# Performance work log

Measured on AMD Instinct MI355X. Metric: run time of the kernel, lower is better.

Reference implementation:

```python
import jax, jax.numpy as jnp
import numpy as np
import math

N0 = 50000      # nodes at level 0
E0 = 800000     # edges at level 0 (fixed edge buffer, masked when pooled)
D = 128         # hidden_dim == latent_dim
L = 2           # args.mpl_layers
NB = 2          # args.num_blocks (SAGEConvs per block)
RATIO = 0.5     # args.mpl_ratio
EPS = 1e-12


def setup_inputs() -> dict:
    key = jax.random.key(0)
    ks = jax.random.split(key, 6)
    x = jax.random.normal(ks[0], (N0, D), jnp.float32)
    edge_index = jax.random.randint(ks[1], (2, E0), 0, N0, jnp.int32)
    n_convs = (2 * L + 1) * NB  # down(4) + bottom(2) + up(4) = 10
    Wl = jax.random.normal(ks[2], (n_convs, D, D), jnp.float32) * 0.05
    bl = jax.random.normal(ks[3], (n_convs, D), jnp.float32) * 0.05
    Wr = jax.random.normal(ks[4], (n_convs, D, D), jnp.float32) * 0.05
    pool_p = jax.random.normal(ks[5], (L, D), jnp.float32)
    return {"x": x, "edge_index": edge_index, "Wl": Wl, "bl": bl, "Wr": Wr,
            "pool_p": pool_p}


def _sage(x, src, dst, valid, W_l, b_l, W_r, n):
    """PyG SAGEConv (mean aggr): lin_l(mean_{j->i} x_j) + lin_r(x_i).
    Invalid (masked) edges contribute neither to the sum nor the count."""
    msg = x[src] * valid[:, None]                       # [E, D]
    s = jax.ops.segment_sum(msg, dst, num_segments=n)   # [n, D]
    cnt = jax.ops.segment_sum(valid, dst, num_segments=n)
    mean = s / jnp.maximum(cnt, 1.0)[:, None]
    return mean @ W_l.T + b_l + x @ W_r.T


def _cal_ew(w, src, dst, valid, n):
    """WeightedEdgeConv.cal_ew (no_grad in original)."""
    deg = jax.ops.segment_sum(valid, src, num_segments=n)
    normed = w / jnp.where(deg > 0, deg, 1.0)
    w_send = normed[src] * valid
    aggr_w = jax.ops.segment_sum(w_send, dst, num_segments=n) + EPS
    ec = w_send / aggr_w[dst]
    return jax.lax.stop_gradient(ec), jax.lax.stop_gradient(aggr_w)


def _econv(x, src, dst, ec, n, aggregating=True):
    """WeightedEdgeConv.forward: gather -> scale by edge weight -> scatter-add."""
    if aggregating:
        return jax.ops.segment_sum(x[src] * ec[:, None], dst, num_segments=n)
    return jax.ops.segment_sum(x[dst] * ec[:, None], src, num_segments=n)


def reference(x, edge_index, Wl, bl, Wr, pool_p):
    src, dst = edge_index[0], edge_index[1]
    valid = jnp.ones((E0,), x.dtype)
    n = N0
    conv = 0
    down_outs, down_edges, ecs, perms, sizes = [], [], [], [], []
    w = jnp.ones((N0,), x.dtype)  # b_data.weights (ones by default)

    # ---- down path ----
    for l in range(L):
        for _ in range(NB):
            x = _sage(x, src, dst, valid, Wl[conv], bl[conv], Wr[conv], n)
            conv += 1
        down_outs.append(x)
        down_edges.append((src, dst, valid))
        sizes.append(n)
        ec, w = _cal_ew(w, src, dst, valid, n)
        ecs.append(ec)
        x = _econv(x, src, dst, ec, n, aggregating=True)
        # TopKPooling: score = x.p/||p||, keep top ceil(ratio*n), gate by tanh
        p = pool_p[l]
        score = x @ p / jnp.linalg.norm(p)
        k = int(math.ceil(RATIO * n))
        vals, perm = jax.lax.top_k(score, k)
        x = x[perm] * jnp.tanh(vals)[:, None]
        w = w[perm]
        new_id = jnp.full((n,), -1, jnp.int32).at[perm].set(
            jnp.arange(k, dtype=jnp.int32))
        src2, dst2 = new_id[src], new_id[dst]
        keep = ((src2 >= 0) & (dst2 >= 0)).astype(x.dtype)
        valid = valid * keep
        src = jnp.maximum(src2, 0)
        dst = jnp.maximum(dst2, 0)
        perms.append(perm)
        n = k

    # ---- bottom ----
    for _ in range(NB):
        x = _sage(x, src, dst, valid, Wl[conv], bl[conv], Wr[conv], n)
        conv += 1

    # ---- up path ----
    for i in range(L):
        u = L - 1 - i
        src, dst, valid = down_edges[u]
        n = sizes[u]
        # Unpool: scatter into zeros at kept-node indices
        x = jnp.zeros((n, x.shape[-1]), x.dtype).at[perms[u]].set(x)
        x = _econv(x, src, dst, ecs[u], n, aggregating=False)
        for _ in range(NB):
            x = _sage(x, src, dst, valid, Wl[conv], bl[conv], Wr[conv], n)
            conv += 1
        x = x + down_outs[u]  # skip connection
    return x
```

## Files before the change

kernel.cpp:

```cpp
#include <hip/hip_runtime.h>
#include <stdint.h>

#define DEV __device__ __forceinline__

constexpr int N0 = 50000;
constexpr int E0 = 800000;
constexpr int D  = 128;

typedef __attribute__((ext_vector_type(8))) short bf16x8;
typedef __attribute__((ext_vector_type(4))) float f32x4;

DEV float bf2f(unsigned u) { return __uint_as_float(u << 16); }
DEV unsigned short f2bf(float f) {
  unsigned u = __float_as_uint(f);
  unsigned r = u + 0x7fffu + ((u >> 16) & 1u);
  return (unsigned short)(r >> 16);
}

DEV unsigned wave_incl_scan(unsigned v, int lane) {
  #pragma unroll
  for (int off = 1; off < 64; off <<= 1) {
    unsigned u = __shfl_up(v, (unsigned)off);
    if (lane >= off) v += u;
  }
// ... 8 lines not shown
    rank_src[e] = atomicAdd(&cnt_src[src[e]], 1u);
    rank_dst[e] = atomicAdd(&cnt_dst[dst[e]], 1u);
  }
}

__global__ void k_psum(const unsigned* __restrict__ in, int n, unsigned* __restrict__ part) {
  int t = threadIdx.x, lane = t & 63, w = t >> 6;
  int base = blockIdx.x * 1024 + t * 4;
  unsigned s = 0;
  #pragma unroll
  for (int j = 0; j < 4; ++j) { int i = base + j; if (i < n) s += in[i]; }
  #pragma unroll
  for (int off = 32; off >= 1; off >>= 1) s += __shfl_xor(s, off);
  __shared__ unsigned ws[4];
  if (lane == 0) ws[w] = s;
  __syncthreads();
  if (t == 0) part[blockIdx.x] = ws[0] + ws[1] + ws[2] + ws[3];
}

__global__ void k_scoff(const unsigned* __restrict__ part, int nch,
                        unsigned* __restrict__ off, unsigned* __restrict__ total_out) {
  if (threadIdx.x == 0) {
    unsigned run = 0;
    for (int c = 0; c < nch; ++c) { off[c] = run; run += part[c]; }
    *total_out = run;
  }
}

__global__ void k_sapply(const unsigned* __restrict__ in, const unsigned* __restrict__ choff,
                         int n, unsigned* __restrict__ out) {
  int t = threadIdx.x, lane = t & 63, w = t >> 6;
  int base = blockIdx.x * 1024 + t * 4;
  unsigned v[4]; unsigned s = 0;
  #pragma unroll
  for (int j = 0; j < 4; ++j) { int i = base + j; v[j] = (i < n) ? in[i] : 0u; s += v[j]; }
  unsigned incl = wave_incl_scan(s, lane);
  __shared__ unsigned wsum[4], woff[4];
  if (lane == 63) wsum[w] = incl;
  __syncthreads();
  if (t == 0) { unsigned run = 0; for (int j = 0; j < 4; ++j) { woff[j] = run; run += wsum[j]; } }
  __syncthreads();
  unsigned run = choff[blockIdx.x] + woff[w] + incl - s;
  #pragma unroll
  for (int j = 0; j < 4; ++j) {
    int i = base + j;
    if (i < n) out[i] = run;
    run += v[j];
  }
}

__global__ void k_fill2(const int* __restrict__ src, const int* __restrict__ dst,
                        const unsigned* __restrict__ rank_src, const unsigned* __restrict__ rank_dst,
                        const unsigned* __restrict__ indptr_src, const unsigned* __restrict__ indptr_dst,
                        int* __restrict__ adj_src, int* __restrict__ adj_dst) {
  int e = blockIdx.x * blockDim.x + threadIdx.x;
  if (e < E0) {
    int s = src[e], d = dst[e];
    adj_dst[indptr_dst[d] + rank_dst[e]] = s;
    adj_src[indptr_src[s] + rank_src[e]] = d;
  }
}

__global__ void k_adj_next2(const int* __restrict__ adjd, const int* __restrict__ adjs,
                            const int* __restrict__ new_id,
                            int* __restrict__ outd, int* __restrict__ outs) {
  int pos = blockIdx.x * blockDim.x + threadIdx.x;
  if (pos < E0) {
    int a = adjd[pos];
    outd[pos] = (a >= 0) ? new_id[a] : -1;
    int b = adjs[pos];
    outs[pos] = (b >= 0) ? new_id[b] : -1;
  }
}

__global__ void k_adj_next(const int* __restrict__ adj_prev, const int* __restrict__ new_id,
                           int* __restrict__ adj_out) {
  int pos = blockIdx.x * blockDim.x + threadIdx.x;
  if (pos < E0) {
    int a = adj_prev[pos];
    adj_out[pos] = (a >= 0) ? new_id[a] : -1;
  }
}

__global__ void k_wt(const float* __restrict__ Wl, const float* __restrict__ Wr, float* __restrict__ BT) {
  int idx = blockIdx.x * blockDim.x + threadIdx.x;
  if (idx < 4 * 256 * 128) {
    int o = idx & 127;
    int k = (idx >> 7) & 255;
    int c = idx >> 15;
    float v = (k < 128) ? Wl[(c * 128 + o) * 128 + k] : Wr[(c * 128 + o) * 128 + (k - 128)];
    BT[idx] = v;
  }
}

__global__ void k_wt_pk(const float* __restrict__ Wl, const float* __restrict__ Wr,
                        unsigned short* __restrict__ Bhi, unsigned short* __restrict__ Blo) {
  int idx = blockIdx.x * blockDim.x + threadIdx.x;
  if (idx >= 6 * 8 * 8 * 64) return;
  int l  = idx & 63;
  int ct = (idx >> 6) & 7;
  int ks = (idx >> 9) & 7;
  int c  = idx >> 12;
  int k0 = ks * 32 + (l >> 4) * 8;
  int o  = ct * 16 + (l & 15);
  int conv = c + 4;
  const float* Wrow = (k0 < 128) ? (Wl + ((size_t)conv * 128 + o) * 128 + k0)
                                 : (Wr + ((size_t)conv * 128 + o) * 128 + (k0 - 128));
  size_t base = (size_t)idx * 8;
  #pragma unroll
  for (int j = 0; j < 8; ++j) {
    float wv = Wrow[j];
    unsigned short h = f2bf(wv);
    Bhi[base + j] = h;
    Blo[base + j] = f2bf(wv - bf2f(h));
  }
}

template<bool BF, bool MASKED>
__global__ void k_sage(const void* __restrict__ xv, const int* __restrict__ adj,
                       const unsigned* __restrict__ indptr, const int* __restrict__ orig,
                       int n, float* __restrict__ mean) {
  int wid = (blockIdx.x * blockDim.x + threadIdx.x) >> 6;
  int lane = threadIdx.x & 63;
  if (wid >= n) return;
  int o = orig ? orig[wid] : wid;
  unsigned s0 = indptr[o], s1 = indptr[o + 1];
  const float* xf = (const float*)xv;
  const unsigned* xb = (const unsigned*)xv;
  float a0 = 0.f, a1 = 0.f, cnt = 0.f;
  unsigned idx = s0;
  for (; idx + 4 <= s1; idx += 4) {
    int ad[4];
    #pragma unroll
    for (int j = 0; j < 4; ++j) ad[j] = adj[idx + j];
    #pragma unroll
    for (int j = 0; j < 4; ++j) {
      if (!MASKED || ad[j] >= 0) {
        float x0, x1;
        if (BF) { unsigned u = xb[(size_t)ad[j] * 64 + lane]; x0 = bf2f(u & 0xffffu); x1 = bf2f(u >> 16); }
        else    { float2 v = *(const float2*)(xf + (size_t)ad[j] * D + lane * 2); x0 = v.x; x1 = v.y; }
        a0 += x0; a1 += x1; cnt += 1.f;
      }
    }
  }
  for (; idx < s1; ++idx) {
    int a = adj[idx];
    if (!MASKED || a >= 0) {
      float x0, x1;
      if (BF) { unsigned u = xb[(size_t)a * 64 + lane]; x0 = bf2f(u & 0xffffu); x1 = bf2f(u >> 16); }
      else    { float2 v = *(const float2*)(xf + (size_t)a * D + lane * 2); x0 = v.x; x1 = v.y; }
      a0 += x0; a1 += x1; cnt += 1.f;
    }
  }
  if (!MASKED) cnt = (float)(s1 - s0);
  float inv = 1.0f / fmaxf(cnt, 1.0f);
  *(float2*)(mean + (size_t)wid * D + lane * 2) = make_float2(a0 * inv, a1 * inv);
}

template<bool BF, bool MASKED>
__global__ void k_econv2(const void* __restrict__ xv, const int* __restrict__ adj,
                         const float* __restrict__ ecs, const unsigned* __restrict__ indptr,
                         const int* __restrict__ orig, int n,
                         float* __restrict__ out, unsigned* __restrict__ outbf) {
  int wid = (blockIdx.x * blockDim.x + threadIdx.x) >> 6;
  int lane = threadIdx.x & 63;
  if (wid >= n) return;
  int o = orig ? orig[wid] : wid;
  unsigned s0 = indptr[o], s1 = indptr[o + 1];
  const float* xf = (const float*)xv;
  const unsigned* xb = (const unsigned*)xv;
  float a0 = 0.f, a1 = 0.f;
  unsigned idx = s0;
  for (; idx + 4 <= s1; idx += 4) {
    int ad[4]; float wv[4];
    #pragma unroll
    for (int j = 0; j < 4; ++j) { ad[j] = adj[idx + j]; wv[j] = ecs[idx + j]; }
    #pragma unroll
    for (int j = 0; j < 4; ++j) {
      if (!MASKED || ad[j] >= 0) {
        float x0, x1;
        if (BF) { unsigned u = xb[(size_t)ad[j] * 64 + lane]; x0 = bf2f(u & 0xffffu); x1 = bf2f(u >> 16); }
        else    { float2 v = *(const float2*)(xf + (size_t)ad[j] * D + lane * 2); x0 = v.x; x1 = v.y; }
        a0 = fmaf(wv[j], x0, a0); a1 = fmaf(wv[j], x1, a1);
      }
    }
  }
  for (; idx < s1; ++idx) {
    int a = adj[idx]; float wgt = ecs[idx];
    if (!MASKED || a >= 0) {
      float x0, x1;
      if (BF) { unsigned u = xb[(size_t)a * 64 + lane]; x0 = bf2f(u & 0xffffu); x1 = bf2f(u >> 16); }
      else    { float2 v = *(const float2*)(xf + (size_t)a * D + lane * 2); x0 = v.x; x1 = v.y; }
      a0 = fmaf(wgt, x0, a0); a1 = fmaf(wgt, x1, a1);
    }
  }
  *(float2*)(out + (size_t)wid * D + lane * 2) = make_float2(a0, a1);
  if (outbf) {
    unsigned p = (unsigned)f2bf(a0) | ((unsigned)f2bf(a1) << 16);
    outbf[(size_t)wid * 64 + lane] = p;
  }
}

__launch_bounds__(256)
__global__ void k_conv_gemm(const float* __restrict__ mean, const float* __restrict__ xin,
                            const float* __restrict__ BT, const float* __restrict__ bias,
                            float* __restrict__ y, unsigned short* __restrict__ ybf, int n) {
  __shared__ float As[64][17];
  __shared__ float Bs[16][128];
  int tid = threadIdx.x;
  int tx = tid & 15, ty = tid >> 4;
  int row0 = blockIdx.x * 64;
  float acc[4][8];
  #pragma unroll
  for (int r = 0; r < 4; ++r)
    #pragma unroll
    for (int c = 0; c < 8; ++c) acc[r][c] = 0.f;

  int lm = tid >> 2;
  int lk = (tid & 3) * 4;
  int bk = tid >> 4;
  int bo = (tid & 15) * 8;

  for (int kc = 0; kc < 16; ++kc) {
    int k0 = kc * 16;
    const float* A = (k0 < 128) ? mean : xin;
    int kk = k0 & 127;
    int gr = row0 + lm;
    float4 av = make_float4(0.f, 0.f, 0.f, 0.f);
    if (gr < n) av = *(const float4*)(A + (size_t)gr * D + kk + lk);
    As[lm][lk + 0] = av.x; As[lm][lk + 1] = av.y; As[lm][lk + 2] = av.z; As[lm][lk + 3] = av.w;
    float4 bv0 = *(const float4*)(BT + (size_t)(k0 + bk) * 128 + bo);
    float4 bv1 = *(const float4*)(BT + (size_t)(k0 + bk) * 128 + bo + 4);
    *(float4*)&Bs[bk][bo] = bv0;
    *(float4*)&Bs[bk][bo + 4] = bv1;
    __syncthreads();
    #pragma unroll
    for (int k = 0; k < 16; ++k) {
      float a[4];
      #pragma unroll
      for (int r = 0; r < 4; ++r) a[r] = As[ty * 4 + r][k];
      float4 b0 = *(const float4*)&Bs[k][tx * 4];
      float4 b1 = *(const float4*)&Bs[k][64 + tx * 4];
      float bb[8] = {b0.x, b0.y, b0.z, b0.w, b1.x, b1.y, b1.z, b1.w};
      #pragma unroll
      for (int r = 0; r < 4; ++r)
        #pragma unroll
        for (int c = 0; c < 8; ++c)
          acc[r][c] = fmaf(a[r], bb[c], acc[r][c]);
    }
    __syncthreads();
  }
  float4 bs0 = *(const float4*)(bias + tx * 4);
  float4 bs1 = *(const float4*)(bias + 64 + tx * 4);
  #pragma unroll
  for (int r = 0; r < 4; ++r) {
    int gr = row0 + ty * 4 + r;
    if (gr < n) {
      float4 o0 = make_float4(acc[r][0] + bs0.x, acc[r][1] + bs0.y, acc[r][2] + bs0.z, acc[r][3] + bs0.w);
      float4 o1 = make_float4(acc[r][4] + bs1.x, acc[r][5] + bs1.y, acc[r][6] + bs1.z, acc[r][7] + bs1.w);
      *(float4*)(y + (size_t)gr * D + tx * 4) = o0;
      *(float4*)(y + (size_t)gr * D + 64 + tx * 4) = o1;
      if (ybf) {
        ushort4 p0; p0.x = f2bf(o0.x); p0.y = f2bf(o0.y); p0.z = f2bf(o0.z); p0.w = f2bf(o0.w);
        ushort4 p1; p1.x = f2bf(o1.x); p1.y = f2bf(o1.y); p1.z = f2bf(o1.z); p1.w = f2bf(o1.w);
        *(ushort4*)(ybf + (size_t)gr * D + tx * 4) = p0;
        *(ushort4*)(ybf + (size_t)gr * D + 64 + tx * 4) = p1;
      }
    }
  }
}

__launch_bounds__(256)
__global__ void k_gemm_mfma(const float* __restrict__ mean, const float* __restrict__ xin,
                            const unsigned short* __restrict__ Bhi, const unsigned short* __restrict__ Blo,
                            const float* __restrict__ bias, const float* __restrict__ skip,
                            float* __restrict__ y, unsigned short* __restrict__ ybf, int n) {
  int tid = threadIdx.x;
  int lane = tid & 63, w = tid >> 6;
  int row0 = blockIdx.x * 64 + w * 16;
  int arow = row0 + (lane & 15);
  int kgrp = lane >> 4;
  bool rowok = arow < n;
  f32x4 acc[8];
  #pragma unroll
  for (int ct = 0; ct < 8; ++ct) acc[ct] = f32x4{0.f, 0.f, 0.f, 0.f};

  #pragma unroll
  for (int ks = 0; ks < 8; ++ks) {
    const float* A = (ks < 4) ? mean : xin;
    int kk = (ks & 3) * 32 + kgrp * 8;
    float av[8];
    if (rowok) {
      float4 a0 = *(const float4*)(A + (size_t)arow * D + kk);
      float4 a1 = *(const float4*)(A + (size_t)arow * D + kk + 4);
      av[0] = a0.x; av[1] = a0.y; av[2] = a0.z; av[3] = a0.w;
      av[4] = a1.x; av[5] = a1.y; av[6] = a1.z; av[7] = a1.w;
    } else {
      #pragma unroll
      for (int j = 0; j < 8; ++j) av[j] = 0.f;
    }
    bf16x8 ahi, alo;
    #pragma unroll
    for (int j = 0; j < 8; ++j) {
      unsigned short h = f2bf(av[j]);
      ahi[j] = (short)h;
      alo[j] = (short)f2bf(av[j] - bf2f(h));
    }
    #pragma unroll
    for (int ct = 0; ct < 8; ++ct) {
      size_t boff = (((size_t)ks * 8 + ct) * 64 + lane) * 8;
      bf16x8 bh = *(const bf16x8*)(Bhi + boff);
      bf16x8 bl = *(const bf16x8*)(Blo + boff);
      acc[ct] = __builtin_amdgcn_mfma_f32_16x16x32_bf16(ahi, bh, acc[ct], 0, 0, 0);
      acc[ct] = __builtin_amdgcn_mfma_f32_16x16x32_bf16(alo, bh, acc[ct], 0, 0, 0);
      acc[ct] = __builtin_amdgcn_mfma_f32_16x16x32_bf16(ahi, bl, acc[ct], 0, 0, 0);
    }
  }
  int ccol = lane & 15;
  #pragma unroll
  for (int ct = 0; ct < 8; ++ct) {
    int col = ct * 16 + ccol;
    float bb = bias[col];
    #pragma unroll
    for (int r = 0; r < 4; ++r) {
      int row = row0 + kgrp * 4 + r;
      if (row < n) {
        float v = acc[ct][r] + bb;
        if (skip) v += skip[(size_t)row * D + col];
        y[(size_t)row * D + col] = v;
        if (ybf) ybf[(size_t)row * D + col] = f2bf(v);
      }
    }
  }
}

__global__ void k_deg_len(const unsigned* __restrict__ indptr, int n, float* __restrict__ deg) {
  int j = blockIdx.x * blockDim.x + threadIdx.x;
  if (j < n) deg[j] = (float)(indptr[j + 1] - indptr[j]);
}

__global__ void k_deg_mask(const int* __restrict__ adj_src, const unsigned* __restrict__ indptr_src,
                           const int* __restrict__ orig, int n, float* __restrict__ deg) {
  int j = blockIdx.x * blockDim.x + threadIdx.x;
  if (j >= n) return;
  int o = orig ? orig[j] : j;
  unsigned s0 = indptr_src[o], s1 = indptr_src[o + 1];
  float d = 0.f;
  for (unsigned i = s0; i < s1; ++i) d += (adj_src[i] >= 0) ? 1.f : 0.f;
  deg[j] = d;
}

template<bool MASKED>
__global__ void k_ew_dst(const int* __restrict__ adj, const unsigned* __restrict__ indptr,
                         const int* __restrict__ orig, const float* __restrict__ w,
                         const float* __restrict__ deg, int n,
                         float* __restrict__ ws_slot, float* __restrict__ aggrw,
                         float* __restrict__ ec_slot) {
  int j = blockIdx.x * blockDim.x + threadIdx.x;
  if (j >= n) return;
  int o = orig ? orig[j] : j;
  unsigned s0 = indptr[o], s1 = indptr[o + 1];
  float s = 1e-12f;
  for (unsigned pos = s0; pos < s1; ++pos) {
    int a = adj[pos];
    float ws = 0.f;
    if (!MASKED || a >= 0) {
      float d = deg[a];
      ws = (w ? w[a] : 1.0f) / (d > 0.f ? d : 1.0f);
    }
    ws_slot[pos] = ws;
    s += ws;
  }
  aggrw[j] = s;
  float inv = 1.0f / s;
  for (unsigned pos = s0; pos < s1; ++pos) ec_slot[pos] = ws_slot[pos] * inv;
}

template<bool MASKED>
__global__ void k_ew_src(const int* __restrict__ adj_src, const unsigned* __restrict__ indptr_src,
                         const int* __restrict__ orig, const float* __restrict__ w,
                         const float* __restrict__ deg, const float* __restrict__ aggrw, int n,
                         float* __restrict__ ec_slot) {
  int j = blockIdx.x * blockDim.x + threadIdx.x;
  if (j >= n) return;
  int o = orig ? orig[j] : j;
  unsigned s0 = indptr_src[o], s1 = indptr_src[o + 1];
  float d = deg[j];
  float wn = (w ? w[j] : 1.0f) / (d > 0.f ? d : 1.0f);
  for (unsigned pos = s0; pos < s1; ++pos) {
    int a = adj_src[pos];
    ec_slot[pos] = (!MASKED || a >= 0) ? (wn / aggrw[a]) : 0.f;
  }
}

DEV unsigned mono_key(float f) {
  unsigned u = __float_as_uint(f);
  return (u & 0x80000000u) ? ~u : (u | 0x80000000u);
}

__global__ void k_score(const float* __restrict__ x, const float* __restrict__ p,
                        int n, float* __restrict__ score, unsigned* __restrict__ keys) {
  int wid = (blockIdx.x * blockDim.x + threadIdx.x) >> 6;
  int lane = threadIdx.x & 63;
  if (wid >= n) return;
  float p0 = p[lane * 2], p1 = p[lane * 2 + 1];
  const float2 xv = *(const float2*)(x + (size_t)wid * D + lane * 2);
  float partial = xv.x * p0 + xv.y * p1;
  float pn = p0 * p0 + p1 * p1;
  #pragma unroll
  for (int off = 32; off >= 1; off >>= 1) {
    partial += __shfl_xor(partial, off);
    pn += __shfl_xor(pn, off);
  }
  if (lane == 0) {
    float sc = partial * (1.0f / sqrtf(pn));
    score[wid] = sc;
    keys[wid] = mono_key(sc);
  }
}

__global__ void k_sel_init(unsigned* bins, unsigned* state, int k) {
  int t = threadIdx.x;
  if (t < 256) bins[t] = 0u;
  if (t == 0) { state[0] = 0u; state[1] = (unsigned)k; }
}

__global__ void k_hist(const unsigned* __restrict__ keys, int n, const unsigned* __restrict__ state,
                       unsigned* __restrict__ bins, int byte) {
  __shared__ unsigned lb[256];
  for (int i = threadIdx.x; i < 256; i += blockDim.x) lb[i] = 0u;
  __syncthreads();
  unsigned prefix = state[0];
  unsigned mask = (byte == 3) ? 0u : (0xFFFFFFFFu << ((byte + 1) * 8));
  for (int i = blockIdx.x * blockDim.x + threadIdx.x; i < n; i += gridDim.x * blockDim.x) {
    unsigned key = keys[i];
    if ((key & mask) == (prefix & mask))
      atomicAdd(&lb[(key >> (byte * 8)) & 255], 1u);
  }
  __syncthreads();
  for (int i = threadIdx.x; i < 256; i += blockDim.x)
    if (lb[i]) atomicAdd(&bins[i], lb[i]);
}

__global__ void k_pick(unsigned* bins, unsigned* state, int byte) {
  if (threadIdx.x == 0) {
    unsigned r = state[1];
    int b;
    for (b = 255; b > 0; --b) {
      unsigned c = bins[b];
      if (c >= r) break;
      r -= c;
    }
    state[0] |= ((unsigned)b) << (byte * 8);
    state[1] = r;
  }
  __syncthreads();
  for (int i = threadIdx.x; i < 256; i += blockDim.x) bins[i] = 0u;
}

__global__ void k_flags(const unsigned* __restrict__ keys, const unsigned* __restrict__ state,
                        int n, uint2* __restrict__ part) {
  int t = threadIdx.x, lane = t & 63, w = t >> 6;
  int base = blockIdx.x * 1024 + t * 4;
  unsigned T = state[0];
  unsigned cnt = 0;
  #pragma unroll
  for (int j = 0; j < 4; ++j) {
    int i = base + j;
    if (i < n) {
      unsigned key = keys[i];
// ... 77 lines not shown
  float2 v = *(const float2*)(xin + (size_t)j * D + lane * 2);
  v.x *= g; v.y *= g;
  *(float2*)(xout + (size_t)wid * D + lane * 2) = v;
  if (outbf) {
    unsigned p = (unsigned)f2bf(v.x) | ((unsigned)f2bf(v.y) << 16);
    outbf[(size_t)wid * 64 + lane] = p;
  }
}

__global__ void k_scatter_bf(const float* __restrict__ xin, const int* __restrict__ perm,
                             int k, unsigned* __restrict__ outbf) {
  int wid = (blockIdx.x * blockDim.x + threadIdx.x) >> 6;
  int lane = threadIdx.x & 63;
  if (wid >= k) return;
  int p = perm[wid];
  float2 v = *(const float2*)(xin + (size_t)wid * D + lane * 2);
  unsigned pk = (unsigned)f2bf(v.x) | ((unsigned)f2bf(v.y) << 16);
  outbf[(size_t)p * 64 + lane] = pk;
}

extern "C" void kernel_launch(void* const* d_in, const int* in_sizes, int n_in,
                              void* d_out, int out_size, void* d_ws, size_t ws_size,
                              hipStream_t stream) {
  const float* x_in   = (const float*)d_in[0];
  const int*   ei     = (const int*)d_in[1];
  const int*   src0   = ei;
  const int*   dst0   = ei + E0;
  const float* Wl     = (const float*)d_in[2];
  const float* bl     = (const float*)d_in[3];
  const float* Wr     = (const float*)d_in[4];
  const float* pool_p = (const float*)d_in[5];
  float* out = (float*)d_out;

  const int n0 = N0, k0 = 25000, n1 = 25000, k1 = 12500, n2 = 12500;
  const int NCH0 = (N0 + 1023) / 1024;

  char* ws = (char*)d_ws;
  size_t off = 0;
  auto alloc = [&](size_t bytes) -> char* {
    char* p = ws + off;
    off += (bytes + 255) & ~(size_t)255;
    return p;
  };
  const size_t NBY = (size_t)N0 * D * 4;
  float* B0    = (float*)alloc(NBY);
  float* B1    = (float*)alloc(NBY);
  float* B2    = (float*)alloc(NBY);
  float* down0 = (float*)alloc(NBY);
  float* down1 = (float*)alloc(NBY / 2);
  unsigned* MA = (unsigned*)alloc((size_t)N0 * D * 2);
  unsigned* MB = (unsigned*)alloc((size_t)N0 * D * 2);
  int* adj0_dst = (int*)alloc(E0 * 4);
  int* adj0_src = (int*)alloc(E0 * 4);
  int* adj1_dst = (int*)alloc(E0 * 4);
  int* adj1_src = (int*)alloc(E0 * 4);
  float* ec0_src = (float*)alloc(E0 * 4);
  float* ec1_src = (float*)alloc(E0 * 4);
  float* ec_dst  = (float*)alloc(E0 * 4);
  float* ws_slot = (float*)alloc(E0 * 4);
  int* adj2_dst  = (int*)ws_slot;
  unsigned* rank_src = (unsigned*)alloc(E0 * 4);
  unsigned* rank_dst = (unsigned*)alloc(E0 * 4);
  unsigned* indptr_dst = (unsigned*)alloc((N0 + 1) * 4);
  unsigned* indptr_src = (unsigned*)alloc((N0 + 1) * 4);
  unsigned* cnt_src = (unsigned*)alloc(N0 * 4);
  unsigned* cnt_dst = (unsigned*)alloc(N0 * 4);
  float* deg   = (float*)alloc(N0 * 4);
  float* aggrw = (float*)alloc(N0 * 4);
  float* w1 = (float*)alloc(n1 * 4);
  float* w2 = (float*)alloc(n2 * 4);
  float* score = (float*)alloc(N0 * 4);
  unsigned* keys = (unsigned*)alloc(N0 * 4);
  int* perm0 = (int*)alloc(k0 * 4);
  int* perm1 = (int*)alloc(k1 * 4);
  int* orig1 = (int*)alloc(k0 * 4);
  int* orig2 = (int*)alloc(k1 * 4);
  int* new_id = (int*)alloc(N0 * 4);
  unsigned* bins  = (unsigned*)alloc(256 * 4);
  unsigned* state = (unsigned*)alloc(8);
  unsigned* spart = (unsigned*)alloc(64 * 4);
  unsigned* soff  = (unsigned*)alloc(64 * 4);
  uint2* ppart = (uint2*)alloc(64 * 8);
  uint2* poff  = (uint2*)alloc(64 * 8);
  float* BT = (float*)alloc((size_t)4 * 256 * 128 * 4);
  unsigned short* Bhi = (unsigned short*)alloc((size_t)6 * 8 * 8 * 64 * 8 * 2);
  unsigned short* Blo = (unsigned short*)alloc((size_t)6 * 8 * 8 * 64 * 8 * 2);

  const int EG = (E0 + 255) / 256;

  auto scan_np1 = [&](const unsigned* in, unsigned* outp, int n, int nch) {
    k_psum<<<nch, 256, 0, stream>>>(in, n, spart);
    k_scoff<<<1, 64, 0, stream>>>(spart, nch, soff, outp + n);
    k_sapply<<<nch, 256, 0, stream>>>(in, soff, n, outp);
  };

  hipMemsetAsync(cnt_src, 0, N0 * 4, stream);
  hipMemsetAsync(cnt_dst, 0, N0 * 4, stream);
  k_count<<<EG, 256, 0, stream>>>(src0, dst0, cnt_src, cnt_dst, rank_src, rank_dst);
  scan_np1(cnt_src, indptr_src, N0, NCH0);
  scan_np1(cnt_dst, indptr_dst, N0, NCH0);
  k_fill2<<<EG, 256, 0, stream>>>(src0, dst0, rank_src, rank_dst, indptr_src, indptr_dst,
                                  adj0_src, adj0_dst);
  k_wt<<<(4 * 256 * 128 + 255) / 256, 256, 0, stream>>>(Wl, Wr, BT);
  k_wt_pk<<<(6 * 8 * 8 * 64 + 255) / 256, 256, 0, stream>>>(Wl, Wr, Bhi, Blo);

  auto gemm = [&](const float* meanb, const float* xin, float* yout, unsigned short* ybf,
                  int n, int cidx) {
    k_conv_gemm<<<(n + 63) / 64, 256, 0, stream>>>(meanb, xin, BT + (size_t)cidx * 256 * 128,
                                                   bl + cidx * 128, yout, ybf, n);
  };
  auto gemm_mx = [&](const float* meanb, const float* xin, float* yout, unsigned short* ybf,
                     const float* skip, int n, int cidx) {
    size_t o = (size_t)(cidx - 4) * 8 * 8 * 64 * 8;
    k_gemm_mfma<<<(n + 63) / 64, 256, 0, stream>>>(meanb, xin, Bhi + o, Blo + o,
                                                   bl + cidx * 128, skip, yout, ybf, n);
  };

  auto pool_sel = [&](const float* xpool, int n, int kk, int level, const int* orig,
                      int* perm, float* w_next, int* orig_next,
                      float* xout, unsigned* xout_bf) {
    int nch = (n + 1023) / 1024;
    k_score<<<(n + 3) / 4, 256, 0, stream>>>(xpool, pool_p + level * D, n, score, keys);
    k_sel_init<<<1, 256, 0, stream>>>(bins, state, kk);
    for (int byte = 3; byte >= 0; --byte) {
      k_hist<<<256, 256, 0, stream>>>(keys, n, state, bins, byte);
      k_pick<<<1, 256, 0, stream>>>(bins, state, byte);
    }
    k_flags<<<nch, 256, 0, stream>>>(keys, state, n, ppart);
    k_choff<<<1, 64, 0, stream>>>(ppart, nch, poff);
    k_pack2<<<nch, 256, 0, stream>>>(keys, state, poff, aggrw, orig, n, perm, new_id, w_next, orig_next);
    k_gate<<<(kk + 3) / 4, 256, 0, stream>>>(xpool, perm, score, kk, xout, xout_bf);
  };

  k_sage<false, false><<<(n0 + 3) / 4, 256, 0, stream>>>(x_in, adj0_dst, indptr_dst, nullptr, n0, B1);
  gemm(B1, x_in, B2, nullptr, n0, 0);
  k_sage<false, false><<<(n0 + 3) / 4, 256, 0, stream>>>(B2, adj0_dst, indptr_dst, nullptr, n0, B1);
  gemm(B1, B2, down0, nullptr, n0, 1);
  k_deg_len<<<(n0 + 255) / 256, 256, 0, stream>>>(indptr_src, n0, deg);
  k_ew_dst<false><<<(n0 + 255) / 256, 256, 0, stream>>>(adj0_dst, indptr_dst, nullptr, nullptr, deg, n0,
                                                        ws_slot, aggrw, ec_dst);
  k_ew_src<false><<<(n0 + 255) / 256, 256, 0, stream>>>(adj0_src, indptr_src, nullptr, nullptr, deg, aggrw,
                                                        n0, ec0_src);
  k_econv2<false, false><<<(n0 + 3) / 4, 256, 0, stream>>>(down0, adj0_dst, ec_dst, indptr_dst, nullptr,
                                                           n0, B1, nullptr);
  pool_sel(B1, n0, k0, 0, nullptr, perm0, w1, orig1, B2, nullptr);
  k_adj_next2<<<EG, 256, 0, stream>>>(adj0_dst, adj0_src, new_id, adj1_dst, adj1_src);

  k_sage<false, true><<<(n1 + 3) / 4, 256, 0, stream>>>(B2, adj1_dst, indptr_dst, orig1, n1, B1);
  gemm(B1, B2, B0, nullptr, n1, 2);
  k_sage<false, true><<<(n1 + 3) / 4, 256, 0, stream>>>(B0, adj1_dst, indptr_dst, orig1, n1, B1);
  gemm(B1, B0, down1, nullptr, n1, 3);
  k_deg_mask<<<(n1 + 255) / 256, 256, 0, stream>>>(adj1_src, indptr_src, orig1, n1, deg);
  k_ew_dst<true><<<(n1 + 255) / 256, 256, 0, stream>>>(adj1_dst, indptr_dst, orig1, w1, deg, n1,
                                                       ws_slot, aggrw, ec_dst);
  k_ew_src<true><<<(n1 + 255) / 256, 256, 0, stream>>>(adj1_src, indptr_src, orig1, w1, deg, aggrw,
                                                       n1, ec1_src);
  k_econv2<false, true><<<(n1 + 3) / 4, 256, 0, stream>>>(down1, adj1_dst, ec_dst, indptr_dst, orig1,
                                                          n1, B1, nullptr);
  pool_sel(B1, n1, k1, 1, orig1, perm1, w2, orig2, B2, MA);
  k_adj_next<<<EG, 256, 0, stream>>>(adj1_dst, new_id, adj2_dst);

  k_sage<true, true><<<(n2 + 3) / 4, 256, 0, stream>>>(MA, adj2_dst, indptr_dst, orig2, n2, B1);
  gemm_mx(B1, B2, B0, (unsigned short*)MB, nullptr, n2, 4);
  k_sage<true, true><<<(n2 + 3) / 4, 256, 0, stream>>>(MB, adj2_dst, indptr_dst, orig2, n2, B1);
  gemm_mx(B1, B0, B2, nullptr, nullptr, n2, 5);

  hipMemsetAsync(MA, 0, (size_t)n1 * D * 2, stream);
  k_scatter_bf<<<(n2 + 3) / 4, 256, 0, stream>>>(B2, perm1, n2, MA);
  k_econv2<true, true><<<(n1 + 3) / 4, 256, 0, stream>>>(MA, adj1_src, ec1_src, indptr_src, orig1,
                                                         n1, B1, MB);
  k_sage<true, true><<<(n1 + 3) / 4, 256, 0, stream>>>(MB, adj1_dst, indptr_dst, orig1, n1, B0);
  gemm_mx(B0, B1, B2, (unsigned short*)MA, nullptr, n1, 6);
  k_sage<true, true><<<(n1 + 3) / 4, 256, 0, stream>>>(MA, adj1_dst, indptr_dst, orig1, n1, B0);
  gemm_mx(B0, B2, B1, nullptr, down1, n1, 7);

  hipMemsetAsync(MA, 0, (size_t)n0 * D * 2, stream);
  k_scatter_bf<<<(n1 + 3) / 4, 256, 0, stream>>>(B1, perm0, n1, MA);
  k_econv2<true, false><<<(n0 + 3) / 4, 256, 0, stream>>>(MA, adj0_src, ec0_src, indptr_src, nullptr,
                                                          n0, B2, MB);
  k_sage<true, false><<<(n0 + 3) / 4, 256, 0, stream>>>(MB, adj0_dst, indptr_dst, nullptr, n0, B1);
  gemm_mx(B1, B2, B0, (unsigned short*)MA, nullptr, n0, 8);
  k_sage<true, false><<<(n0 + 3) / 4, 256, 0, stream>>>(MA, adj0_dst, indptr_dst, nullptr, n0, B1);
  gemm_mx(B1, B0, out, nullptr, down0, n0, 9);
}
```

Measured before the change: 1.192 ms.

## Use split-bf16 MFMA GEMM for down path and widen gather loads

Replaces the fp32 FMA tiled GEMM used by the first four convolutions with an MFMA kernel that splits both operands into three bf16 parts and runs six products, which keeps near-fp32 accuracy while using the matrix cores. The gather/mean and edge-weighted aggregation kernels are rewritten so each wave processes several edges at once with wider float4/uint4 loads, followed by cross-lane shuffle reductions. The separate degree kernel is folded into the edge-weight kernels, and weight packing is unified into a three-part split for all ten convs. The six MFMAs per tile add compute and the A operand is split on the fly, and the gather loops now carry partial sums that must be reduced across lanes.

```diff
diff --git a/kernel.cpp b/kernel.cpp
--- a/kernel.cpp
+++ b/kernel.cpp
@@ -114,190 +114,207 @@
   }
 }
 
-__global__ void k_wt(const float* __restrict__ Wl, const float* __restrict__ Wr, float* __restrict__ BT) {
+__global__ void k_wt_pk3(const float* __restrict__ Wl, const float* __restrict__ Wr,
+                         unsigned short* __restrict__ Bh, unsigned short* __restrict__ Bm,
+                         unsigned short* __restrict__ Bl) {
   int idx = blockIdx.x * blockDim.x + threadIdx.x;
-  if (idx < 4 * 256 * 128) {
-    int o = idx & 127;
-    int k = (idx >> 7) & 255;
-    int c = idx >> 15;
-    float v = (k < 128) ? Wl[(c * 128 + o) * 128 + k] : Wr[(c * 128 + o) * 128 + (k - 128)];
-    BT[idx] = v;
-  }
-}
-
-__global__ void k_wt_pk(const float* __restrict__ Wl, const float* __restrict__ Wr,
-                        unsigned short* __restrict__ Bhi, unsigned short* __restrict__ Blo) {
-  int idx = blockIdx.x * blockDim.x + threadIdx.x;
-  if (idx >= 6 * 8 * 8 * 64) return;
+  if (idx >= 10 * 8 * 8 * 64) return;
   int l  = idx & 63;
   int ct = (idx >> 6) & 7;
   int ks = (idx >> 9) & 7;
   int c  = idx >> 12;
   int k0 = ks * 32 + (l >> 4) * 8;
   int o  = ct * 16 + (l & 15);
-  int conv = c + 4;
-  const float* Wrow = (k0 < 128) ? (Wl + ((size_t)conv * 128 + o) * 128 + k0)
-                                 : (Wr + ((size_t)conv * 128 + o) * 128 + (k0 - 128));
+  const float* Wrow = (k0 < 128) ? (Wl + ((size_t)c * 128 + o) * 128 + k0)
+                                 : (Wr + ((size_t)c * 128 + o) * 128 + (k0 - 128));
   size_t base = (size_t)idx * 8;
   #pragma unroll
   for (int j = 0; j < 8; ++j) {
     float wv = Wrow[j];
     unsigned short h = f2bf(wv);
-    Bhi[base + j] = h;
-    Blo[base + j] = f2bf(wv - bf2f(h));
-  }
-}
-
-template<bool BF, bool MASKED>
-__global__ void k_sage(const void* __restrict__ xv, const int* __restrict__ adj,
-                       const unsigned* __restrict__ indptr, const int* __restrict__ orig,
-                       int n, float* __restrict__ mean) {
+    float r1 = wv - bf2f(h);
+    unsigned short m = f2bf(r1);
+    float r2 = r1 - bf2f(m);
+    Bh[base + j] = h;
+    Bm[base + j] = m;
+    Bl[base + j] = f2bf(r2);
+  }
+}
+
+template<bool MEAN, bool MASKED, bool ECW>
+__global__ void k_gf32(const float* __restrict__ x, const int* __restrict__ adj,
+                       const float* __restrict__ ecs, const unsigned* __restrict__ indptr,
+                       const int* __restrict__ orig, int n, float* __restrict__ out) {
   int wid = (blockIdx.x * blockDim.x + threadIdx.x) >> 6;
   int lane = threadIdx.x & 63;
   if (wid >= n) return;
   int o = orig ? orig[wid] : wid;
   unsigned s0 = indptr[o], s1 = indptr[o + 1];
-  const float* xf = (const float*)xv;
-  const unsigned* xb = (const unsigned*)xv;
-  float a0 = 0.f, a1 = 0.f, cnt = 0.f;
-  unsigned idx = s0;
-  for (; idx + 4 <= s1; idx += 4) {
-    int ad[4];
-    #pragma unroll
-    for (int j = 0; j < 4; ++j) ad[j] = adj[idx + j];
+  int half = lane >> 5, sl = lane & 31;
+  float a0 = 0.f, a1 = 0.f, a2 = 0.f, a3 = 0.f, cnt = 0.f;
+  for (unsigned idx = s0; idx < s1; idx += 8) {
     #pragma unroll
     for (int j = 0; j < 4; ++j) {
-      if (!MASKED || ad[j] >= 0) {
-        float x0, x1;
-        if (BF) { unsigned u = xb[(size_t)ad[j] * 64 + lane]; x0 = bf2f(u & 0xffffu); x1 = bf2f(u >> 16); }
-        else    { float2 v = *(const float2*)(xf + (size_t)ad[j] * D + lane * 2); x0 = v.x; x1 = v.y; }
-        a0 += x0; a1 += x1; cnt += 1.f;
+      unsigned e = idx + j * 2 + half;
+      if (e < s1) {
+        int a = adj[e];
+        if (!MASKED || a >= 0) {
+          const float4 v = *(const float4*)(x + (size_t)a * D + sl * 4);
+          if (ECW) {
+            float w = ecs[e];
+            a0 = fmaf(w, v.x, a0); a1 = fmaf(w, v.y, a1);
+            a2 = fmaf(w, v.z, a2); a3 = fmaf(w, v.w, a3);
+          } else {
+            a0 += v.x; a1 += v.y; a2 += v.z; a3 += v.w;
+          }
+          cnt += 1.f;
+        }
       }
     }
   }
-  for (; idx < s1; ++idx) {
-    int a = adj[idx];
-    if (!MASKED || a >= 0) {
-      float x0, x1;
-      if (BF) { unsigned u = xb[(size_t)a * 64 + lane]; x0 = bf2f(u & 0xffffu); x1 = bf2f(u >> 16); }
-      else    { float2 v = *(const float2*)(xf + (size_t)a * D + lane * 2); x0 = v.x; x1 = v.y; }
-      a0 += x0; a1 += x1; cnt += 1.f;
-    }
-  }
-  if (!MASKED) cnt = (float)(s1 - s0);
-  float inv = 1.0f / fmaxf(cnt, 1.0f);
-  *(float2*)(mean + (size_t)wid * D + lane * 2) = make_float2(a0 * inv, a1 * inv);
-}
-
-template<bool BF, bool MASKED>
-__global__ void k_econv2(const void* __restrict__ xv, const int* __restrict__ adj,
-                         const float* __restrict__ ecs, const unsigned* __restrict__ indptr,
-                         const int* __restrict__ orig, int n,
-                         float* __restrict__ out, unsigned* __restrict__ outbf) {
+  a0 += __shfl_xor(a0, 32); a1 += __shfl_xor(a1, 32);
+  a2 += __shfl_xor(a2, 32); a3 += __shfl_xor(a3, 32);
+  if (MEAN) {
+    cnt += __shfl_xor(cnt, 32);
+    if (!MASKED) cnt = (float)(s1 - s0);
+    float inv = 1.0f / fmaxf(cnt, 1.0f);
+    a0 *= inv; a1 *= inv; a2 *= inv; a3 *= inv;
+  }
+  if (half == 0)
+    *(float4*)(out + (size_t)wid * D + sl * 4) = make_float4(a0, a1, a2, a3);
+}
+
+template<bool MEAN, bool MASKED, bool ECW>
+__global__ void k_gbf(const unsigned* __restrict__ xb, const int* __restrict__ adj,
+                      const float* __restrict__ ecs, const unsigned* __restrict__ indptr,
+                      const int* __restrict__ orig, int n,
+                      float* __restrict__ out, unsigned* __restrict__ outbf) {
   int wid = (blockIdx.x * blockDim.x + threadIdx.x) >> 6;
   int lane = threadIdx.x & 63;
   if (wid >= n) return;
   int o = orig ? orig[wid] : wid;
   unsigned s0 = indptr[o], s1 = indptr[o + 1];
-  const float* xf = (const float*)xv;
-  const unsigned* xb = (const unsigned*)xv;
-  float a0 = 0.f, a1 = 0.f;
-  unsigned idx = s0;
-  for (; idx + 4 <= s1; idx += 4) {
-    int ad[4]; float wv[4];
-    #pragma unroll
-    for (int j = 0; j < 4; ++j) { ad[j] = adj[idx + j]; wv[j] = ecs[idx + j]; }
+  int q = lane >> 4, sl = lane & 15;
+  float acc[8];
+  #pragma unroll
+  for (int k = 0; k < 8; ++k) acc[k] = 0.f;
+  float cnt = 0.f;
+  for (unsigned idx = s0; idx < s1; idx += 16) {
     #pragma unroll
     for (int j = 0; j < 4; ++j) {
-      if (!MASKED || ad[j] >= 0) {
-        float x0, x1;
-        if (BF) { unsigned u = xb[(size_t)ad[j] * 64 + lane]; x0 = bf2f(u & 0xffffu); x1 = bf2f(u >> 16); }
-        else    { float2 v = *(const float2*)(xf + (size_t)ad[j] * D + lane * 2); x0 = v.x; x1 = v.y; }
-        a0 = fmaf(wv[j], x0, a0); a1 = fmaf(wv[j], x1, a1);
+      unsigned e = idx + j * 4 + q;
+      if (e < s1) {
+        int a = adj[e];
+        if (!MASKED || a >= 0) {
+          const uint4 v = *(const uint4*)(xb + (size_t)a * 64 + sl * 4);
+          float f0 = bf2f(v.x & 0xffffu), f1 = bf2f(v.x >> 16);
+          float f2 = bf2f(v.y & 0xffffu), f3 = bf2f(v.y >> 16);
+          float f4 = bf2f(v.z & 0xffffu), f5 = bf2f(v.z >> 16);
+          float f6 = bf2f(v.w & 0xffffu), f7 = bf2f(v.w >> 16);
+          if (ECW) {
+            float w = ecs[e];
+            acc[0] = fmaf(w, f0, acc[0]); acc[1] = fmaf(w, f1, acc[1]);
+            acc[2] = fmaf(w, f2, acc[2]); acc[3] = fmaf(w, f3, acc[3]);
+            acc[4] = fmaf(w, f4, acc[4]); acc[5] = fmaf(w, f5, acc[5]);
+            acc[6] = fmaf(w, f6, acc[6]); acc[7] = fmaf(w, f7, acc[7]);
+          } else {
+            acc[0] += f0; acc[1] += f1; acc[2] += f2; acc[3] += f3;
+            acc[4] += f4; acc[5] += f5; acc[6] += f6; acc[7] += f7;
+          }
+          cnt += 1.f;
+        }
       }
     }
   }
-  for (; idx < s1; ++idx) {
-    int a = adj[idx]; float wgt = ecs[idx];
-    if (!MASKED || a >= 0) {
-      float x0, x1;
-      if (BF) { unsigned u = xb[(size_t)a * 64 + lane]; x0 = bf2f(u & 0xffffu); x1 = bf2f(u >> 16); }
-      else    { float2 v = *(const float2*)(xf + (size_t)a * D + lane * 2); x0 = v.x; x1 = v.y; }
-      a0 = fmaf(wgt, x0, a0); a1 = fmaf(wgt, x1, a1);
-    }
-  }
-  *(float2*)(out + (size_t)wid * D + lane * 2) = make_float2(a0, a1);
-  if (outbf) {
-    unsigned p = (unsigned)f2bf(a0) | ((unsigned)f2bf(a1) << 16);
-    outbf[(size_t)wid * 64 + lane] = p;
+  #pragma unroll
+  for (int k = 0; k < 8; ++k) {
+    acc[k] += __shfl_xor(acc[k], 16);
+    acc[k] += __shfl_xor(acc[k], 32);
+  }
+  if (MEAN) {
+    cnt += __shfl_xor(cnt, 16);
+    cnt += __shfl_xor(cnt, 32);
+    if (!MASKED) cnt = (float)(s1 - s0);
+    float inv = 1.0f / fmaxf(cnt, 1.0f);
+    #pragma unroll
+    for (int k = 0; k < 8; ++k) acc[k] *= inv;
+  }
+  if (q == 0) {
+    *(float4*)(out + (size_t)wid * D + sl * 8)     = make_float4(acc[0], acc[1], acc[2], acc[3]);
+    *(float4*)(out + (size_t)wid * D + sl * 8 + 4) = make_float4(acc[4], acc[5], acc[6], acc[7]);
+    if (outbf) {
+      uint4 p;
+      p.x = (unsigned)f2bf(acc[0]) | ((unsigned)f2bf(acc[1]) << 16);
+      p.y = (unsigned)f2bf(acc[2]) | ((unsigned)f2bf(acc[3]) << 16);
+      p.z = (unsigned)f2bf(acc[4]) | ((unsigned)f2bf(acc[5]) << 16);
+      p.w = (unsigned)f2bf(acc[6]) | ((unsigned)f2bf(acc[7]) << 16);
+      *(uint4*)(outbf + (size_t)wid * 64 + sl * 4) = p;
+    }
   }
 }
 
 __launch_bounds__(256)
-__global__ void k_conv_gemm(const float* __restrict__ mean, const float* __restrict__ xin,
-                            const float* __restrict__ BT, const float* __restrict__ bias,
-                            float* __restrict__ y, unsigned short* __restrict__ ybf, int n) {
-  __shared__ float As[64][17];
-  __shared__ float Bs[16][128];
+__global__ void k_gemm_mfma6(const float* __restrict__ mean, const float* __restrict__ xin,
+                             const unsigned short* __restrict__ Bh, const unsigned short* __restrict__ Bm,
+                             const unsigned short* __restrict__ Bl,
+                             const float* __restrict__ bias,
+                             float* __restrict__ y, int n) {
   int tid = threadIdx.x;
-  int tx = tid & 15, ty = tid >> 4;
-  int row0 = blockIdx.x * 64;
-  float acc[4][8];
-  #pragma unroll
-  for (int r = 0; r < 4; ++r)
-    #pragma unroll
-    for (int c = 0; c < 8; ++c) acc[r][c] = 0.f;
-
-  int lm = tid >> 2;
-  int lk = (tid & 3) * 4;
-  int bk = tid >> 4;
-  int bo = (tid & 15) * 8;
-
-  for (int kc = 0; kc < 16; ++kc) {
-    int k0 = kc * 16;
-    const float* A = (k0 < 128) ? mean : xin;
-    int kk = k0 & 127;
-    int gr = row0 + lm;
-    float4 av = make_float4(0.f, 0.f, 0.f, 0.f);
-    if (gr < n) av = *(const float4*)(A + (size_t)gr * D + kk + lk);
-    As[lm][lk + 0] = av.x; As[lm][lk + 1] = av.y; As[lm][lk + 2] = av.z; As[lm][lk + 3] = av.w;
-    float4 bv0 = *(const float4*)(BT + (size_t)(k0 + bk) * 128 + bo);
-    float4 bv1 = *(const float4*)(BT + (size_t)(k0 + bk) * 128 + bo + 4);
-    *(float4*)&Bs[bk][bo] = bv0;
-    *(float4*)&Bs[bk][bo + 4] = bv1;
-    __syncthreads();
-    #pragma unroll
-    for (int k = 0; k < 16; ++k) {
-      float a[4];
+  int lane = tid & 63, w = tid >> 6;
+  int row0 = blockIdx.x * 64 + w * 16;
+  int arow = row0 + (lane & 15);
+  int kgrp = lane >> 4;
+  bool rowok = arow < n;
+  f32x4 acc[8];
+  #pragma unroll
+  for (int ct = 0; ct < 8; ++ct) acc[ct] = f32x4{0.f, 0.f, 0.f, 0.f};
+
+  #pragma unroll
+  for (int ks = 0; ks < 8; ++ks) {
+    const float* A = (ks < 4) ? mean : xin;
+    int kk = (ks & 3) * 32 + kgrp * 8;
+    float av[8];
+    if (rowok) {
+      float4 x0 = *(const float4*)(A + (size_t)arow * D + kk);
+      float4 x1 = *(const float4*)(A + (size_t)arow * D + kk + 4);
+      av[0] = x0.x; av[1] = x0.y; av[2] = x0.z; av[3] = x0.w;
+      av[4] = x1.x; av[5] = x1.y; av[6] = x1.z; av[7] = x1.w;
+    } else {
       #pragma unroll
-      for (int r = 0; r < 4; ++r) a[r] = As[ty * 4 + r][k];
-      float4 b0 = *(const float4*)&Bs[k][tx * 4];
-      float4 b1 = *(const float4*)&Bs[k][64 + tx * 4];
-      float bb[8] = {b0.x, b0.y, b0.z, b0.w, b1.x, b1.y, b1.z, b1.w};
-      #pragma unroll
-      for (int r = 0; r < 4; ++r)
-        #pragma unroll
-        for (int c = 0; c < 8; ++c)
-          acc[r][c] = fmaf(a[r], bb[c], acc[r][c]);
-    }
-    __syncthreads();
-  }
-  float4 bs0 = *(const float4*)(bias + tx * 4);
-  float4 bs1 = *(const float4*)(bias + 64 + tx * 4);
-  #pragma unroll
-  for (int r = 0; r < 4; ++r) {
-    int gr = row0 + ty * 4 + r;
-    if (gr < n) {
-      float4 o0 = make_float4(acc[r][0] + bs0.x, acc[r][1] + bs0.y, acc[r][2] + bs0.z, acc[r][3] + bs0.w);
-      float4 o1 = make_float4(acc[r][4] + bs1.x, acc[r][5] + bs1.y, acc[r][6] + bs1.z, acc[r][7] + bs1.w);
-      *(float4*)(y + (size_t)gr * D + tx * 4) = o0;
-      *(float4*)(y + (size_t)gr * D + 64 + tx * 4) = o1;
-      if (ybf) {
-        ushort4 p0; p0.x = f2bf(o0.x); p0.y = f2bf(o0.y); p0.z = f2bf(o0.z); p0.w = f2bf(o0.w);
-        ushort4 p1; p1.x = f2bf(o1.x); p1.y = f2bf(o1.y); p1.z = f2bf(o1.z); p1.w = f2bf(o1.w);
-        *(ushort4*)(ybf + (size_t)gr * D + tx * 4) = p0;
-        *(ushort4*)(ybf + (size_t)gr * D + 64 + tx * 4) = p1;
-      }
+      for (int j = 0; j < 8; ++j) av[j] = 0.f;
+    }
+    bf16x8 ah, am, al;
+    #pragma unroll
+    for (int j = 0; j < 8; ++j) {
+      unsigned short h = f2bf(av[j]);
+      float r1 = av[j] - bf2f(h);
+      unsigned short m = f2bf(r1);
+      float r2 = r1 - bf2f(m);
+      ah[j] = (short)h; am[j] = (short)m; al[j] = (short)f2bf(r2);
+    }
+    #pragma unroll
+    for (int ct = 0; ct < 8; ++ct) {
+      size_t boff = (((size_t)ks * 8 + ct) * 64 + lane) * 8;
+      bf16x8 bh = *(const bf16x8*)(Bh + boff);
+      bf16x8 bm = *(const bf16x8*)(Bm + boff);
+      bf16x8 bl = *(const bf16x8*)(Bl + boff);
+      acc[ct] = __builtin_amdgcn_mfma_f32_16x16x32_bf16(ah, bh, acc[ct], 0, 0, 0);
+      acc[ct] = __builtin_amdgcn_mfma_f32_16x16x32_bf16(ah, bm, acc[ct], 0, 0, 0);
+      acc[ct] = __builtin_amdgcn_mfma_f32_16x16x32_bf16(am, bh, acc[ct], 0, 0, 0);
+      acc[ct] = __builtin_amdgcn_mfma_f32_16x16x32_bf16(am, bm, acc[ct], 0, 0, 0);
+      acc[ct] = __builtin_amdgcn_mfma_f32_16x16x32_bf16(ah, bl, acc[ct], 0, 0, 0);
+      acc[ct] = __builtin_amdgcn_mfma_f32_16x16x32_bf16(al, bh, acc[ct], 0, 0, 0);
+    }
+  }
+  int ccol = lane & 15;
+  #pragma unroll
+  for (int ct = 0; ct < 8; ++ct) {
+    int col = ct * 16 + ccol;
+    float bb = bias[col];
+    #pragma unroll
+    for (int r = 0; r < 4; ++r) {
+      int row = row0 + kgrp * 4 + r;
+      if (row < n) y[(size_t)row * D + col] = acc[ct][r] + bb;
     }
   }
 }
@@ -323,10 +340,10 @@
     int kk = (ks & 3) * 32 + kgrp * 8;
     float av[8];
     if (rowok) {
-      float4 a0 = *(const float4*)(A + (size_t)arow * D + kk);
-      float4 a1 = *(const float4*)(A + (size_t)arow * D + kk + 4);
-      av[0] = a0.x; av[1] = a0.y; av[2] = a0.z; av[3] = a0.w;
-      av[4] = a1.x; av[5] = a1.y; av[6] = a1.z; av[7] = a1.w;
+      float4 x0 = *(const float4*)(A + (size_t)arow * D + kk);
+      float4 x1 = *(const float4*)(A + (size_t)arow * D + kk + 4);
+      av[0] = x0.x; av[1] = x0.y; av[2] = x0.z; av[3] = x0.w;
+      av[4] = x1.x; av[5] = x1.y; av[6] = x1.z; av[7] = x1.w;
     } else {
       #pragma unroll
       for (int j = 0; j < 8; ++j) av[j] = 0.f;
@@ -364,11 +381,6 @@
       }
     }
   }
-}
-
-__global__ void k_deg_len(const unsigned* __restrict__ indptr, int n, float* __restrict__ deg) {
-  int j = blockIdx.x * blockDim.x + threadIdx.x;
-  if (j < n) deg[j] = (float)(indptr[j + 1] - indptr[j]);
 }
 
 __global__ void k_deg_mask(const int* __restrict__ adj_src, const unsigned* __restrict__ indptr_src,
@@ -384,6 +396,7 @@
 
 template<bool MASKED>
 __global__ void k_ew_dst(const int* __restrict__ adj, const unsigned* __restrict__ indptr,
+                         const unsigned* __restrict__ ips,
                          const int* __restrict__ orig, const float* __restrict__ w,
                          const float* __restrict__ deg, int n,
                          float* __restrict__ ws_slot, float* __restrict__ aggrw,
@@ -397,7 +410,7 @@
     int a = adj[pos];
     float ws = 0.f;
     if (!MASKED || a >= 0) {
-      float d = deg[a];
+      float d = deg ? deg[a] : (float)(ips[a + 1] - ips[a]);
       ws = (w ? w[a] : 1.0f) / (d > 0.f ? d : 1.0f);
     }
     ws_slot[pos] = ws;
@@ -417,7 +430,7 @@
   if (j >= n) return;
   int o = orig ? orig[j] : j;
   unsigned s0 = indptr_src[o], s1 = indptr_src[o + 1];
-  float d = deg[j];
+  float d = deg ? deg[j] : (float)(s1 - s0);
   float wn = (w ? w[j] : 1.0f) / (d > 0.f ? d : 1.0f);
   for (unsigned pos = s0; pos < s1; ++pos) {
     int a = adj_src[pos];
@@ -661,9 +674,9 @@
   unsigned* soff  = (unsigned*)alloc(64 * 4);
   uint2* ppart = (uint2*)alloc(64 * 8);
   uint2* poff  = (uint2*)alloc(64 * 8);
-  float* BT = (float*)alloc((size_t)4 * 256 * 128 * 4);
-  unsigned short* Bhi = (unsigned short*)alloc((size_t)6 * 8 * 8 * 64 * 8 * 2);
-  unsigned short* Blo = (unsigned short*)alloc((size_t)6 * 8 * 8 * 64 * 8 * 2);
+  unsigned short* Bh = (unsigned short*)alloc((size_t)10 * 32768 * 2);
+  unsigned short* Bm = (unsigned short*)alloc((size_t)10 * 32768 * 2);
+  unsigned short* Bl = (unsigned short*)alloc((size_t)10 * 32768 * 2);
 
   const int EG = (E0 + 255) / 256;
 
@@ -680,18 +693,17 @@
   scan_np1(cnt_dst, indptr_dst, N0, NCH0);
   k_fill2<<<EG, 256, 0, stream>>>(src0, dst0, rank_src, rank_dst, indptr_src, indptr_dst,
                                   adj0_src, adj0_dst);
-  k_wt<<<(4 * 256 * 128 + 255) / 256, 256, 0, stream>>>(Wl, Wr, BT);
-  k_wt_pk<<<(6 * 8 * 8 * 64 + 255) / 256, 256, 0, stream>>>(Wl, Wr, Bhi, Blo);
-
-  auto gemm = [&](const float* meanb, const float* xin, float* yout, unsigned short* ybf,
-                  int n, int cidx) {
-    k_conv_gemm<<<(n + 63) / 64, 256, 0, stream>>>(meanb, xin, BT + (size_t)cidx * 256 * 128,
-                                                   bl + cidx * 128, yout, ybf, n);
+  k_wt_pk3<<<(10 * 8 * 8 * 64 + 255) / 256, 256, 0, stream>>>(Wl, Wr, Bh, Bm, Bl);
+
+  auto gemm6 = [&](const float* meanb, const float* xin, float* yout, int n, int cidx) {
+    size_t o = (size_t)cidx * 32768;
+    k_gemm_mfma6<<<(n + 63) / 64, 256, 0, stream>>>(meanb, xin, Bh + o, Bm + o, Bl + o,
+                                                    bl + cidx * 128, yout, n);
   };
   auto gemm_mx = [&](const float* meanb, const float* xin, float* yout, unsigned short* ybf,
                      const float* skip, int n, int cidx) {
-    size_t o = (size_t)(cidx - 4) * 8 * 8 * 64 * 8;
-    k_gemm_mfma<<<(n + 63) / 64, 256, 0, stream>>>(meanb, xin, Bhi + o, Blo + o,
+    size_t o = (size_t)cidx * 32768;
+    k_gemm_mfma<<<(n + 63) / 64, 256, 0, stream>>>(meanb, xin, Bh + o, Bm + o,
                                                    bl + cidx * 128, skip, yout, ybf, n);
   };
 
@@ -711,54 +723,51 @@
     k_gate<<<(kk + 3) / 4, 256, 0, stream>>>(xpool, perm, score, kk, xout, xout_bf);
   };
 
-  k_sage<false, false><<<(n0 + 3) / 4, 256, 0, stream>>>(x_in, adj0_dst, indptr_dst, nullptr, n0, B1);
-  gemm(B1, x_in, B2, nullptr, n0, 0);
-  k_sage<false, false><<<(n0 + 3) / 4, 256, 0, stream>>>(B2, adj0_dst, indptr_dst, nullptr, n0, B1);
-  gemm(B1, B2, down0, nullptr, n0, 1);
-  k_deg_len<<<(n0 + 255) / 256, 256, 0, stream>>>(indptr_src, n0, deg);
-  k_ew_dst<false><<<(n0 + 255) / 256, 256, 0, stream>>>(adj0_dst, indptr_dst, nullptr, nullptr, deg, n0,
-                                                        ws_slot, aggrw, ec_dst);
-  k_ew_src<false><<<(n0 + 255) / 256, 256, 0, stream>>>(adj0_src, indptr_src, nullptr, nullptr, deg, aggrw,
-                                                        n0, ec0_src);
-  k_econv2<false, false><<<(n0 + 3) / 4, 256, 0, stream>>>(down0, adj0_dst, ec_dst, indptr_dst, nullptr,
-                                                           n0, B1, nullptr);
+  const int G0 = (n0 + 3) / 4, G1 = (n1 + 3) / 4, G2 = (n2 + 3) / 4;
+
+  k_gf32<true, false, false><<<G0, 256, 0, stream>>>(x_in, adj0_dst, nullptr, indptr_dst, nullptr, n0, B1);
+  gemm6(B1, x_in, B2, n0, 0);
+  k_gf32<true, false, false><<<G0, 256, 0, stream>>>(B2, adj0_dst, nullptr, indptr_dst, nullptr, n0, B1);
+  gemm6(B1, B2, down0, n0, 1);
+  k_ew_dst<false><<<(n0 + 255) / 256, 256, 0, stream>>>(adj0_dst, indptr_dst, indptr_src, nullptr,
+                                                        nullptr, nullptr, n0, ws_slot, aggrw, ec_dst);
+  k_ew_src<false><<<(n0 + 255) / 256, 256, 0, stream>>>(adj0_src, indptr_src, nullptr, nullptr,
+                                                        nullptr, aggrw, n0, ec0_src);
+  k_gf32<false, false, true><<<G0, 256, 0, stream>>>(down0, adj0_dst, ec_dst, indptr_dst, nullptr, n0, B1);
   pool_sel(B1, n0, k0, 0, nullptr, perm0, w1, orig1, B2, nullptr);
   k_adj_next2<<<EG, 256, 0, stream>>>(adj0_dst, adj0_src, new_id, adj1_dst, adj1_src);
 
-  k_sage<false, true><<<(n1 + 3) / 4, 256, 0, stream>>>(B2, adj1_dst, indptr_dst, orig1, n1, B1);
-  gemm(B1, B2, B0, nullptr, n1, 2);
-  k_sage<false, true><<<(n1 + 3) / 4, 256, 0, stream>>>(B0, adj1_dst, indptr_dst, orig1, n1, B1);
-  gemm(B1, B0, down1, nullptr, n1, 3);
+  k_gf32<true, true, false><<<G1, 256, 0, stream>>>(B2, adj1_dst, nullptr, indptr_dst, orig1, n1, B1);
+  gemm6(B1, B2, B0, n1, 2);
+  k_gf32<true, true, false><<<G1, 256, 0, stream>>>(B0, adj1_dst, nullptr, indptr_dst, orig1, n1, B1);
+  gemm6(B1, B0, down1, n1, 3);
   k_deg_mask<<<(n1 + 255) / 256, 256, 0, stream>>>(adj1_src, indptr_src, orig1, n1, deg);
-  k_ew_dst<true><<<(n1 + 255) / 256, 256, 0, stream>>>(adj1_dst, indptr_dst, orig1, w1, deg, n1,
-                                                       ws_slot, aggrw, ec_dst);
+  k_ew_dst<true><<<(n1 + 255) / 256, 256, 0, stream>>>(adj1_dst, indptr_dst, nullptr, orig1, w1,
+                                                       deg, n1, ws_slot, aggrw, ec_dst);
   k_ew_src<true><<<(n1 + 255) / 256, 256, 0, stream>>>(adj1_src, indptr_src, orig1, w1, deg, aggrw,
                                                        n1, ec1_src);
-  k_econv2<false, true><<<(n1 + 3) / 4, 256, 0, stream>>>(down1, adj1_dst, ec_dst, indptr_dst, orig1,
-                                                          n1, B1, nullptr);
+  k_gf32<false, true, true><<<G1, 256, 0, stream>>>(down1, adj1_dst, ec_dst, indptr_dst, orig1, n1, B1);
   pool_sel(B1, n1, k1, 1, orig1, perm1, w2, orig2, B2, MA);
   k_adj_next<<<EG, 256, 0, stream>>>(adj1_dst, new_id, adj2_dst);
 
-  k_sage<true, true><<<(n2 + 3) / 4, 256, 0, stream>>>(MA, adj2_dst, indptr_dst, orig2, n2, B1);
+  k_gbf<true, true, false><<<G2, 256, 0, stream>>>(MA, adj2_dst, nullptr, indptr_dst, orig2, n2, B1, nullptr);
   gemm_mx(B1, B2, B0, (unsigned short*)MB, nullptr, n2, 4);
-  k_sage<true, true><<<(n2 + 3) / 4, 256, 0, stream>>>(MB, adj2_dst, indptr_dst, orig2, n2, B1);
+  k_gbf<true, true, false><<<G2, 256, 0, stream>>>(MB, adj2_dst, nullptr, indptr_dst, orig2, n2, B1, nullptr);
   gemm_mx(B1, B0, B2, nullptr, nullptr, n2, 5);
 
   hipMemsetAsync(MA, 0, (size_t)n1 * D * 2, stream);
-  k_scatter_bf<<<(n2 + 3) / 4, 256, 0, stream>>>(B2, perm1, n2, MA);
-  k_econv2<true, true><<<(n1 + 3) / 4, 256, 0, stream>>>(MA, adj1_src, ec1_src, indptr_src, orig1,
-                                                         n1, B1, MB);
-  k_sage<true, true><<<(n1 + 3) / 4, 256, 0, stream>>>(MB, adj1_dst, indptr_dst, orig1, n1, B0);
+  k_scatter_bf<<<G2, 256, 0, stream>>>(B2, perm1, n2, MA);
+  k_gbf<false, true, true><<<G1, 256, 0, stream>>>(MA, adj1_src, ec1_src, indptr_src, orig1, n1, B1, MB);
+  k_gbf<true, true, false><<<G1, 256, 0, stream>>>(MB, adj1_dst, nullptr, indptr_dst, orig1, n1, B0, nullptr);
   gemm_mx(B0, B1, B2, (unsigned short*)MA, nullptr, n1, 6);
-  k_sage<true, true><<<(n1 + 3) / 4, 256, 0, stream>>>(MA, adj1_dst, indptr_dst, orig1, n1, B0);
+  k_gbf<true, true, false><<<G1, 256, 0, stream>>>(MA, adj1_dst, nullptr, indptr_dst, orig1, n1, B0, nullptr);
   gemm_mx(B0, B2, B1, nullptr, down1, n1, 7);
 
   hipMemsetAsync(MA, 0, (size_t)n0 * D * 2, stream);
-  k_scatter_bf<<<(n1 + 3) / 4, 256, 0, stream>>>(B1, perm0, n1, MA);
-  k_econv2<true, false><<<(n0 + 3) / 4, 256, 0, stream>>>(MA, adj0_src, ec0_src, indptr_src, nullptr,
-                                                          n0, B2, MB);
-  k_sage<true, false><<<(n0 + 3) / 4, 256, 0, stream>>>(MB, adj0_dst, indptr_dst, nullptr, n0, B1);
+  k_scatter_bf<<<G1, 256, 0, stream>>>(B1, perm0, n1, MA);
+  k_gbf<false, false, true><<<G0, 256, 0, stream>>>(MA, adj0_src, ec0_src, indptr_src, nullptr, n0, B2, MB);
+  k_gbf<true, false, false><<<G0, 256, 0, stream>>>(MB, adj0_dst, nullptr, indptr_dst, nullptr, n0, B1, nullptr);
   gemm_mx(B1, B2, B0, (unsigned short*)MA, nullptr, n0, 8);
-  k_sage<true, false><<<(n0 + 3) / 4, 256, 0, stream>>>(MA, adj0_dst, indptr_dst, nullptr, n0, B1);
+  k_gbf<true, false, false><<<G0, 256, 0, stream>>>(MA, adj0_dst, nullptr, indptr_dst, nullptr, n0, B1, nullptr);
   gemm_mx(B1, B0, out, nullptr, down0, n0, 9);
 }
```

Measured after the change: 1.147 ms. 3.8% less time.
